# Kernel optimization log

Measured on AMD Instinct MI355X. Metric: run time of the kernel, lower is better.

The kernel has to match this reference:

```python
import jax, jax.numpy as jnp
import numpy as np

N, E, B = 100000, 3200000, 64   # nodes, edges, graphs
F_IN, F_OUT, N_OUT = 20, 20, 5


def setup_inputs() -> dict:
    key = jax.random.key(0)
    ks = jax.random.split(key, 9)
    x = jax.random.normal(ks[0], (N, F_IN), jnp.float32)
    edge_index = jax.random.randint(ks[1], (2, E), 0, N, dtype=jnp.int32)
    batch = jnp.sort(jax.random.randint(ks[2], (N,), 0, B, dtype=jnp.int32))
    s = 1.0 / np.sqrt(F_IN)
    W = jax.random.normal(ks[3], (F_IN, F_OUT), jnp.float32) * s       # GAT linear
    att_src = jax.random.normal(ks[4], (F_OUT,), jnp.float32) * s      # a_src (heads=1)
    att_dst = jax.random.normal(ks[5], (F_OUT,), jnp.float32) * s      # a_dst
    bias = jax.random.normal(ks[6], (F_OUT,), jnp.float32) * 0.01
    out_W = jax.random.normal(ks[7], (F_OUT, N_OUT), jnp.float32) * s
    out_b = jax.random.normal(ks[8], (N_OUT,), jnp.float32) * 0.01
    return {"x": x, "edge_index": edge_index, "batch": batch, "W": W,
            "att_src": att_src, "att_dst": att_dst, "bias": bias,
            "out_W": out_W, "out_b": out_b}


def reference(x, edge_index, batch, W, att_src, att_dst, bias, out_W, out_b):
    n = x.shape[0]
    # PyG GATConv default: add self-loops
    loop = jnp.arange(n, dtype=edge_index.dtype)
    src = jnp.concatenate([edge_index[0], loop])
    dst = jnp.concatenate([edge_index[1], loop])

    h = x @ W                                   # [N, F_OUT]
    a_s = h @ att_src                           # [N]
    a_d = h @ att_dst                           # [N]
    # per-edge attention logit, LeakyReLU(0.2) as in PyG GATConv
    e = jax.nn.leaky_relu(a_s[src] + a_d[dst], negative_slope=0.2)
    # segment softmax over incoming edges of each destination node
    m = jax.ops.segment_max(e, dst, num_segments=n)
    ex = jnp.exp(e - m[dst])
    den = jax.ops.segment_sum(ex, dst, num_segments=n)
    alpha = ex / den[dst]                       # [E+N]  (dropout inactive in eval)
    agg = jax.ops.segment_sum(alpha[:, None] * h[src], dst, num_segments=n) + bias

    xact = jax.nn.leaky_relu(agg, negative_slope=0.01)   # nn.LeakyReLU default
    # global mean pool per graph
    cnt = jax.ops.segment_sum(jnp.ones((n,), xact.dtype), batch, num_segments=B)
    pooled = jax.ops.segment_sum(xact, batch, num_segments=B) / jnp.maximum(cnt, 1.0)[:, None]
    logits = pooled @ out_W + out_b             # [B, 5]
    return jax.nn.softmax(logits, axis=-1)
```

## Files before the change

kernel.cpp:

```cpp
#include <hip/hip_runtime.h>
#include <math.h>

#define F_IN 20
#define F_OUT 20
#define N_OUT 5
#define NPB 128
#define NPB_SH 7
#define NBLK_A 256
#define HS 24
#define CAPMAX 5632
#define NBUCKMAX 800

__global__ __launch_bounds__(1024) void k1a_fused(
    const float* __restrict__ x, const float* __restrict__ W,
    const float* __restrict__ att_s, const float* __restrict__ att_d,
    float* __restrict__ hpack, float* __restrict__ a_d,
    const int* __restrict__ ei, int* __restrict__ gcur,
    unsigned int* __restrict__ bdata,
    int n, int E, int nbuck, int cap, int k1blocks)
{
    __shared__ float sW[F_IN * F_OUT];
    __shared__ float sas[F_OUT];
    __shared__ float sad[F_OUT];
    __shared__ int   sh[3 * NBUCKMAX];

    int tid = threadIdx.x;

    if (blockIdx.x < k1blocks) {
        for (int i = tid; i < F_IN * F_OUT; i += 1024) sW[i] = W[i];
        if (tid < F_OUT) { sas[tid] = att_s[tid]; sad[tid] = att_d[tid]; }
        __syncthreads();

        int i = blockIdx.x * 1024 + tid;
        if (i >= n) return;

        float xi[F_IN];
        const float4* xp = (const float4*)(x + (size_t)i * F_IN);
#pragma unroll
        for (int q = 0; q < F_IN / 4; ++q) {
            float4 v = xp[q];
            xi[4 * q + 0] = v.x; xi[4 * q + 1] = v.y;
            xi[4 * q + 2] = v.z; xi[4 * q + 3] = v.w;
        }

        float hrow[F_OUT];
        float as_acc = 0.f, ad_acc = 0.f;
#pragma unroll
        for (int j = 0; j < F_OUT; ++j) {
            float hj = 0.f;
#pragma unroll
            for (int k = 0; k < F_IN; ++k) hj += xi[k] * sW[k * F_OUT + j];
            hrow[j] = hj;
            as_acc += hj * sas[j];
            ad_acc += hj * sad[j];
        }

        float4* hp = (float4*)(hpack + (size_t)i * HS);
#pragma unroll
        for (int q = 0; q < F_OUT / 4; ++q) {
            float4 v;
            v.x = hrow[4 * q + 0]; v.y = hrow[4 * q + 1];
            v.z = hrow[4 * q + 2]; v.w = hrow[4 * q + 3];
            hp[q] = v;
        }
        float4 tail; tail.x = as_acc; tail.y = 0.f; tail.z = 0.f; tail.w = 0.f;
        hp[5] = tail;
        a_d[i] = ad_acc;
    } else {
        int bb   = blockIdx.x - k1blocks;
        int nbb  = gridDim.x - k1blocks;
        int* hist = sh;
        int* base = sh + nbuck;
        int* cur  = sh + 2 * nbuck;
        for (int b = tid; b < nbuck; b += 1024) { hist[b] = 0; cur[b] = 0; }
        __syncthreads();

        int chunk = (E + nbb - 1) / nbb;
        int start = bb * chunk;
        int end   = min(E, start + chunk);
        const int* dsts = ei + E;

        for (int e = start + tid; e < end; e += 1024)
            atomicAdd(&hist[dsts[e] >> NPB_SH], 1);
        __syncthreads();

        for (int b = tid; b < nbuck; b += 1024) {
            int c = hist[b];
            base[b] = c ? atomicAdd(&gcur[b], c) : 0;
        }
        __syncthreads();

        for (int e = start + tid; e < end; e += 1024) {
            int d = dsts[e];
            int s = ei[e];
            int b = d >> NPB_SH;
            int pos = base[b] + atomicAdd(&cur[b], 1);
            if (pos < cap)
                bdata[(size_t)b * cap + pos] =
                    ((unsigned)s << NPB_SH) | (unsigned)(d & (NPB - 1));
        }
    }
}

__global__ __launch_bounds__(512) void kb_srt(const int* __restrict__ gcur,
                                              const unsigned int* __restrict__ bdata,
                                              const float* __restrict__ hpack,
                                              const float* __restrict__ a_d,
                                              const float* __restrict__ bias,
                                              float* __restrict__ xact,
                                              int n, int cap)
{
    __shared__ int   sent[CAPMAX];
    __shared__ int   hist[NPB];
    __shared__ int   incl[NPB];
    __shared__ int   cur[NPB];
    __shared__ float adl[NPB];
    __shared__ float sbias[F_OUT];

    int b = blockIdx.x;
    int node_lo = b << NPB_SH;
    int nn = min(NPB, n - node_lo);
    int tid = threadIdx.x;

    if (tid < NPB) { hist[tid] = 0; cur[tid] = 0; }
    if (tid < nn) adl[tid] = a_d[node_lo + tid];
    if (tid < F_OUT) sbias[tid] = bias[tid];
    __syncthreads();

    int cnt = min(gcur[b], cap);
    const unsigned int* bd = bdata + (size_t)b * cap;

    for (int e = tid; e < cnt; e += 512)
        atomicAdd(&hist[bd[e] & (NPB - 1)], 1);
    __syncthreads();

    if (tid < NPB) incl[tid] = hist[tid];
    __syncthreads();
#pragma unroll
    for (int s = 1; s < NPB; s <<= 1) {
        int v = 0;
        if (tid < NPB && tid >= s) v = incl[tid - s];
        __syncthreads();
        if (tid < NPB) incl[tid] += v;
        __syncthreads();
    }

    for (int e = tid; e < cnt; e += 512) {
        unsigned w = bd[e];
        int ldst = (int)(w & (NPB - 1));
        int pos = incl[ldst] - hist[ldst] + atomicAdd(&cur[ldst], 1);
        sent[pos] = (int)(w >> NPB_SH);
    }
    __syncthreads();

    int node = tid >> 2, sub = tid & 3;
    float acc[21];
#pragma unroll
    for (int f = 0; f < 21; ++f) acc[f] = 0.f;

    if (node < nn) {
        int start = incl[node] - hist[node];
        int end   = incl[node];
        float ad  = adl[node];
        for (int k = start + sub; k < end; k += 4) {
            int src = sent[k];
            const float* row = hpack + (size_t)src * HS;
            const float4* hp = (const float4*)row;
            float as = row[20];
            float vv = as + ad;
            vv = vv > 0.f ? vv : 0.2f * vv;
            float ex = __expf(vv);
            float4 h0 = hp[0], h1 = hp[1], h2 = hp[2], h3 = hp[3], h4 = hp[4];
            acc[0]  += ex * h0.x; acc[1]  += ex * h0.y;
            acc[2]  += ex * h0.z; acc[3]  += ex * h0.w;
            acc[4]  += ex * h1.x; acc[5]  += ex * h1.y;
            acc[6]  += ex * h1.z; acc[7]  += ex * h1.w;
            acc[8]  += ex * h2.x; acc[9]  += ex * h2.y;
            acc[10] += ex * h2.z; acc[11] += ex * h2.w;
            acc[12] += ex * h3.x; acc[13] += ex * h3.y;
            acc[14] += ex * h3.z; acc[15] += ex * h3.w;
            acc[16] += ex * h4.x; acc[17] += ex * h4.y;
            acc[18] += ex * h4.z; acc[19] += ex * h4.w;
            acc[20] += ex;
        }
    }

#pragma unroll
    for (int f = 0; f < 21; ++f) {
        acc[f] += __shfl_xor(acc[f], 1);
        acc[f] += __shfl_xor(acc[f], 2);
    }

    if (node < nn && sub == 0) {
        int i = node_lo + node;
        const float* row = hpack + (size_t)i * HS;
        float vv = row[20] + adl[node];
        vv = vv > 0.f ? vv : 0.2f * vv;
        float exs = __expf(vv);
        float inv = 1.f / (acc[20] + exs);

        const float4* hp = (const float4*)row;
        float4* op = (float4*)(xact + (size_t)i * F_OUT);
#pragma unroll
        for (int q = 0; q < F_OUT / 4; ++q) {
            float4 hv = hp[q];
            float t0 = (acc[4 * q + 0] + exs * hv.x) * inv + sbias[4 * q + 0];
            float t1 = (acc[4 * q + 1] + exs * hv.y) * inv + sbias[4 * q + 1];
            float t2 = (acc[4 * q + 2] + exs * hv.z) * inv + sbias[4 * q + 2];
            float t3 = (acc[4 * q + 3] + exs * hv.w) * inv + sbias[4 * q + 3];
            float4 o;
            o.x = t0 > 0.f ? t0 : 0.01f * t0;
            o.y = t1 > 0.f ? t1 : 0.01f * t1;
            o.z = t2 > 0.f ? t2 : 0.01f * t2;
            o.w = t3 > 0.f ? t3 : 0.01f * t3;
            op[q] = o;
        }
    }
}

__global__ void k3_pool(const float* __restrict__ xact, const int* __restrict__ batch,
                        float* __restrict__ pooled, int n)
{
    int b = blockIdx.x;
    __shared__ int s_bounds[2];
    __shared__ float partial[4][F_OUT];
    if (threadIdx.x < 2) {
        int target = b + threadIdx.x;
        int lo = 0, hi = n;
        while (lo < hi) {
            int m = (lo + hi) >> 1;
            if (batch[m] < target) lo = m + 1; else hi = m;
        }
        s_bounds[threadIdx.x] = lo;
    }
    __syncthreads();
    int start = s_bounds[0], end = s_bounds[1];

    float acc[F_OUT];
#pragma unroll
    for (int f = 0; f < F_OUT; ++f) acc[f] = 0.f;

    for (int i = start + (int)threadIdx.x; i < end; i += (int)blockDim.x) {
        const float4* ap = (const float4*)(xact + (size_t)i * F_OUT);
#pragma unroll
        for (int q = 0; q < F_OUT / 4; ++q) {
            float4 v = ap[q];
            acc[4 * q + 0] += v.x;
            acc[4 * q + 1] += v.y;
            acc[4 * q + 2] += v.z;
            acc[4 * q + 3] += v.w;
        }
    }

#pragma unroll
    for (int f = 0; f < F_OUT; ++f) {
        float v = acc[f];
        v += __shfl_down(v, 32);
        v += __shfl_down(v, 16);
        v += __shfl_down(v, 8);
        v += __shfl_down(v, 4);
        v += __shfl_down(v, 2);
        v += __shfl_down(v, 1);
        acc[f] = v;
    }
    int wave = threadIdx.x >> 6, lane = threadIdx.x & 63;
    if (lane == 0) {
#pragma unroll
        for (int f = 0; f < F_OUT; ++f) partial[wave][f] = acc[f];
    }
    __syncthreads();
    if (threadIdx.x < F_OUT) {
        int f = threadIdx.x;
        float sum = partial[0][f] + partial[1][f] + partial[2][f] + partial[3][f];
        float cnt = (float)(end - start);
        cnt = cnt > 1.f ? cnt : 1.f;
        pooled[b * F_OUT + f] = sum / cnt;
    }
}

__global__ void k4_head(const float* __restrict__ pooled, const float* __restrict__ out_W,
                        const float* __restrict__ out_b, float* __restrict__ out, int B)
{
    int g = blockIdx.x * blockDim.x + threadIdx.x;
    if (g >= B) return;
    float p[F_OUT];
#pragma unroll
    for (int f = 0; f < F_OUT; ++f) p[f] = pooled[g * F_OUT + f];
    float lg[N_OUT];
#pragma unroll
    for (int o = 0; o < N_OUT; ++o) {
        float acc = out_b[o];
#pragma unroll
        for (int f = 0; f < F_OUT; ++f) acc += p[f] * out_W[f * N_OUT + o];
        lg[o] = acc;
    }
    float m = lg[0];
#pragma unroll
    for (int o = 1; o < N_OUT; ++o) m = lg[o] > m ? lg[o] : m;
    float s = 0.f;
#pragma unroll
    for (int o = 0; o < N_OUT; ++o) { lg[o] = expf(lg[o] - m); s += lg[o]; }
    float inv = 1.f / s;
#pragma unroll
    for (int o = 0; o < N_OUT; ++o) out[g * N_OUT + o] = lg[o] * inv;
}

extern "C" void kernel_launch(void* const* d_in, const int* in_sizes, int n_in,
                              void* d_out, int out_size, void* d_ws, size_t ws_size,
                              hipStream_t stream)
{
    const float* x       = (const float*)d_in[0];
    const int*   ei      = (const int*)  d_in[1];
    const int*   batch   = (const int*)  d_in[2];
    const float* W       = (const float*)d_in[3];
    const float* att_src = (const float*)d_in[4];
    const float* att_dst = (const float*)d_in[5];
    const float* bias    = (const float*)d_in[6];
    const float* out_W   = (const float*)d_in[7];
    const float* out_b   = (const float*)d_in[8];
    float* out = (float*)d_out;

    int n = in_sizes[0] / F_IN;
    int E = in_sizes[1] / 2;
    int B = out_size / N_OUT;

    int nbuck = (n + NPB - 1) >> NPB_SH;
    int avg   = E / nbuck;
    int cap   = avg + avg / 4 + 256;
    if (cap > CAPMAX) cap = CAPMAX;

    char* ws = (char*)d_ws;
    float* hpack  = (float*)ws;        ws += (size_t)n * HS * 4;
    float* a_d    = (float*)ws;        ws += (size_t)n * 4;
    float* xact   = (float*)ws;        ws += (size_t)n * F_OUT * 4;
    float* pooled = (float*)ws;        ws += (size_t)B * F_OUT * 4;
    int*   gcur   = (int*)ws;          ws += (size_t)nbuck * 4;
    ws = (char*)(((size_t)ws + 15) & ~(size_t)15);
    unsigned int* bdata = (unsigned int*)ws;  ws += (size_t)nbuck * cap * 4;

    hipMemsetAsync(gcur, 0, (size_t)nbuck * 4, stream);

    int k1blocks = (n + 1023) / 1024;

    k1a_fused<<<k1blocks + NBLK_A, 1024, 0, stream>>>(
        x, W, att_src, att_dst, hpack, a_d, ei, gcur, bdata,
        n, E, nbuck, cap, k1blocks);
    kb_srt   <<<nbuck, 512, 0, stream>>>(gcur, bdata, hpack, a_d, bias, xact, n, cap);
    k3_pool  <<<B, 256, 0, stream>>>(xact, batch, pooled, n);
    k4_head  <<<1, 64, 0, stream>>>(pooled, out_W, out_b, out, B);
}
```

Before: 202.3 us.

## Pack node features as bf16 and fuse mean-pooling into aggregation kernel

Node features h are stored as packed bf16 pairs with the fp32 source attention logit in a 64-byte row, down from a 96-byte fp32 row. This cuts the bytes fetched per edge in the random gather. The pooling kernel is removed: the aggregation kernel accumulates activations per graph in shared memory and atomically adds them to a global pooled buffer, and the head kernel divides by node counts. This drops the xact write and read-back and one launch, at the cost of bf16 rounding of h and nondeterministic float atomic ordering.

```diff
diff --git a/kernel.cpp b/kernel.cpp
--- a/kernel.cpp
+++ b/kernel.cpp
@@ -7,14 +7,25 @@
 #define NPB 128
 #define NPB_SH 7
 #define NBLK_A 256
-#define HS 24
+#define HSW 16
 #define CAPMAX 5632
 #define NBUCKMAX 800
+#define SPMAX 8
+
+__device__ __forceinline__ unsigned pack2bf(float a, float b) {
+    unsigned ua = __float_as_uint(a);
+    unsigned ub = __float_as_uint(b);
+    ua = (ua + 0x7fffu + ((ua >> 16) & 1u)) >> 16;
+    ub = ((ub + 0x7fffu + ((ub >> 16) & 1u)) >> 16) << 16;
+    return ua | ub;
+}
+#define BF2LO(u) __uint_as_float((u) << 16)
+#define BF2HI(u) __uint_as_float((u) & 0xffff0000u)
 
 __global__ __launch_bounds__(1024) void k1a_fused(
     const float* __restrict__ x, const float* __restrict__ W,
     const float* __restrict__ att_s, const float* __restrict__ att_d,
-    float* __restrict__ hpack, float* __restrict__ a_d,
+    unsigned* __restrict__ hpack, float* __restrict__ a_d,
     const int* __restrict__ ei, int* __restrict__ gcur,
     unsigned int* __restrict__ bdata,
     int n, int E, int nbuck, int cap, int k1blocks)
@@ -55,16 +66,21 @@
             ad_acc += hj * sad[j];
         }
 
-        float4* hp = (float4*)(hpack + (size_t)i * HS);
-#pragma unroll
-        for (int q = 0; q < F_OUT / 4; ++q) {
-            float4 v;
-            v.x = hrow[4 * q + 0]; v.y = hrow[4 * q + 1];
-            v.z = hrow[4 * q + 2]; v.w = hrow[4 * q + 3];
+        unsigned rw[HSW];
+#pragma unroll
+        for (int j = 0; j < 10; ++j) rw[j] = pack2bf(hrow[2 * j], hrow[2 * j + 1]);
+        rw[10] = __float_as_uint(as_acc);
+#pragma unroll
+        for (int j = 11; j < HSW; ++j) rw[j] = 0u;
+
+        uint4* hp = (uint4*)(hpack + (size_t)i * HSW);
+#pragma unroll
+        for (int q = 0; q < HSW / 4; ++q) {
+            uint4 v;
+            v.x = rw[4 * q + 0]; v.y = rw[4 * q + 1];
+            v.z = rw[4 * q + 2]; v.w = rw[4 * q + 3];
             hp[q] = v;
         }
-        float4 tail; tail.x = as_acc; tail.y = 0.f; tail.z = 0.f; tail.w = 0.f;
-        hp[5] = tail;
         a_d[i] = ad_acc;
     } else {
         int bb   = blockIdx.x - k1blocks;
@@ -104,10 +120,11 @@
 
 __global__ __launch_bounds__(512) void kb_srt(const int* __restrict__ gcur,
                                               const unsigned int* __restrict__ bdata,
-                                              const float* __restrict__ hpack,
+                                              const unsigned* __restrict__ hpack,
                                               const float* __restrict__ a_d,
                                               const float* __restrict__ bias,
-                                              float* __restrict__ xact,
+                                              const int* __restrict__ batch,
+                                              float* __restrict__ pooled,
                                               int n, int cap)
 {
     __shared__ int   sent[CAPMAX];
@@ -115,7 +132,9 @@
     __shared__ int   incl[NPB];
     __shared__ int   cur[NPB];
     __shared__ float adl[NPB];
+    __shared__ int   sbatch[NPB];
     __shared__ float sbias[F_OUT];
+    __shared__ float spool[SPMAX * F_OUT];
 
     int b = blockIdx.x;
     int node_lo = b << NPB_SH;
@@ -123,8 +142,12 @@
     int tid = threadIdx.x;
 
     if (tid < NPB) { hist[tid] = 0; cur[tid] = 0; }
-    if (tid < nn) adl[tid] = a_d[node_lo + tid];
+    if (tid < nn) {
+        adl[tid] = a_d[node_lo + tid];
+        sbatch[tid] = batch[node_lo + tid];
+    }
     if (tid < F_OUT) sbias[tid] = bias[tid];
+    if (tid < SPMAX * F_OUT) spool[tid] = 0.f;
     __syncthreads();
 
     int cnt = min(gcur[b], cap);
@@ -164,23 +187,22 @@
         float ad  = adl[node];
         for (int k = start + sub; k < end; k += 4) {
             int src = sent[k];
-            const float* row = hpack + (size_t)src * HS;
-            const float4* hp = (const float4*)row;
-            float as = row[20];
+            const uint4* rp = (const uint4*)(hpack + (size_t)src * HSW);
+            uint4 r0 = rp[0], r1 = rp[1], r2 = rp[2];
+            float as = __uint_as_float(r2.z);
             float vv = as + ad;
             vv = vv > 0.f ? vv : 0.2f * vv;
             float ex = __expf(vv);
-            float4 h0 = hp[0], h1 = hp[1], h2 = hp[2], h3 = hp[3], h4 = hp[4];
-            acc[0]  += ex * h0.x; acc[1]  += ex * h0.y;
-            acc[2]  += ex * h0.z; acc[3]  += ex * h0.w;
-            acc[4]  += ex * h1.x; acc[5]  += ex * h1.y;
-            acc[6]  += ex * h1.z; acc[7]  += ex * h1.w;
-            acc[8]  += ex * h2.x; acc[9]  += ex * h2.y;
-            acc[10] += ex * h2.z; acc[11] += ex * h2.w;
-            acc[12] += ex * h3.x; acc[13] += ex * h3.y;
-            acc[14] += ex * h3.z; acc[15] += ex * h3.w;
-            acc[16] += ex * h4.x; acc[17] += ex * h4.y;
-            acc[18] += ex * h4.z; acc[19] += ex * h4.w;
+            acc[0]  += ex * BF2LO(r0.x); acc[1]  += ex * BF2HI(r0.x);
+            acc[2]  += ex * BF2LO(r0.y); acc[3]  += ex * BF2HI(r0.y);
+            acc[4]  += ex * BF2LO(r0.z); acc[5]  += ex * BF2HI(r0.z);
+            acc[6]  += ex * BF2LO(r0.w); acc[7]  += ex * BF2HI(r0.w);
+            acc[8]  += ex * BF2LO(r1.x); acc[9]  += ex * BF2HI(r1.x);
+            acc[10] += ex * BF2LO(r1.y); acc[11] += ex * BF2HI(r1.y);
+            acc[12] += ex * BF2LO(r1.z); acc[13] += ex * BF2HI(r1.z);
+            acc[14] += ex * BF2LO(r1.w); acc[15] += ex * BF2HI(r1.w);
+            acc[16] += ex * BF2LO(r2.x); acc[17] += ex * BF2HI(r2.x);
+            acc[18] += ex * BF2LO(r2.y); acc[19] += ex * BF2HI(r2.y);
             acc[20] += ex;
         }
     }
@@ -193,99 +215,75 @@
 
     if (node < nn && sub == 0) {
         int i = node_lo + node;
-        const float* row = hpack + (size_t)i * HS;
-        float vv = row[20] + adl[node];
+        const uint4* rp = (const uint4*)(hpack + (size_t)i * HSW);
+        uint4 r0 = rp[0], r1 = rp[1], r2 = rp[2];
+        float vv = __uint_as_float(r2.z) + adl[node];
         vv = vv > 0.f ? vv : 0.2f * vv;
         float exs = __expf(vv);
         float inv = 1.f / (acc[20] + exs);
 
-        const float4* hp = (const float4*)row;
-        float4* op = (float4*)(xact + (size_t)i * F_OUT);
-#pragma unroll
-        for (int q = 0; q < F_OUT / 4; ++q) {
-            float4 hv = hp[q];
-            float t0 = (acc[4 * q + 0] + exs * hv.x) * inv + sbias[4 * q + 0];
-            float t1 = (acc[4 * q + 1] + exs * hv.y) * inv + sbias[4 * q + 1];
-            float t2 = (acc[4 * q + 2] + exs * hv.z) * inv + sbias[4 * q + 2];
-            float t3 = (acc[4 * q + 3] + exs * hv.w) * inv + sbias[4 * q + 3];
-            float4 o;
-            o.x = t0 > 0.f ? t0 : 0.01f * t0;
-            o.y = t1 > 0.f ? t1 : 0.01f * t1;
-            o.z = t2 > 0.f ? t2 : 0.01f * t2;
-            o.w = t3 > 0.f ? t3 : 0.01f * t3;
-            op[q] = o;
-        }
-    }
-}
-
-__global__ void k3_pool(const float* __restrict__ xact, const int* __restrict__ batch,
-                        float* __restrict__ pooled, int n)
+        float hs[F_OUT];
+        hs[0]  = BF2LO(r0.x); hs[1]  = BF2HI(r0.x);
+        hs[2]  = BF2LO(r0.y); hs[3]  = BF2HI(r0.y);
+        hs[4]  = BF2LO(r0.z); hs[5]  = BF2HI(r0.z);
+        hs[6]  = BF2LO(r0.w); hs[7]  = BF2HI(r0.w);
+        hs[8]  = BF2LO(r1.x); hs[9]  = BF2HI(r1.x);
+        hs[10] = BF2LO(r1.y); hs[11] = BF2HI(r1.y);
+        hs[12] = BF2LO(r1.z); hs[13] = BF2HI(r1.z);
+        hs[14] = BF2LO(r1.w); hs[15] = BF2HI(r1.w);
+        hs[16] = BF2LO(r2.x); hs[17] = BF2HI(r2.x);
+        hs[18] = BF2LO(r2.y); hs[19] = BF2HI(r2.y);
+
+        float v[F_OUT];
+#pragma unroll
+        for (int f = 0; f < F_OUT; ++f) {
+            float t = (acc[f] + exs * hs[f]) * inv + sbias[f];
+            v[f] = t > 0.f ? t : 0.01f * t;
+        }
+
+        int gl = sbatch[node] - sbatch[0];
+        if (gl < SPMAX) {
+#pragma unroll
+            for (int f = 0; f < F_OUT; ++f) atomicAdd(&spool[gl * F_OUT + f], v[f]);
+        } else {
+#pragma unroll
+            for (int f = 0; f < F_OUT; ++f)
+                atomicAdd(&pooled[(size_t)sbatch[node] * F_OUT + f], v[f]);
+        }
+    }
+    __syncthreads();
+
+    int g0 = sbatch[0];
+    int ngl = min(SPMAX, sbatch[nn - 1] - g0 + 1);
+    for (int idx = tid; idx < ngl * F_OUT; idx += 512)
+        atomicAdd(&pooled[(size_t)(g0 + idx / F_OUT) * F_OUT + idx % F_OUT], spool[idx]);
+}
+
+__global__ void k4_head(const float* __restrict__ pooled, const int* __restrict__ batch,
+                        const float* __restrict__ out_W, const float* __restrict__ out_b,
+                        float* __restrict__ out, int B, int n)
 {
-    int b = blockIdx.x;
-    __shared__ int s_bounds[2];
-    __shared__ float partial[4][F_OUT];
-    if (threadIdx.x < 2) {
-        int target = b + threadIdx.x;
+    int g = blockIdx.x * blockDim.x + threadIdx.x;
+    if (g >= B) return;
+
+    int bnd[2];
+#pragma unroll
+    for (int t = 0; t < 2; ++t) {
+        int target = g + t;
         int lo = 0, hi = n;
         while (lo < hi) {
             int m = (lo + hi) >> 1;
             if (batch[m] < target) lo = m + 1; else hi = m;
         }
-        s_bounds[threadIdx.x] = lo;
-    }
-    __syncthreads();
-    int start = s_bounds[0], end = s_bounds[1];
-
-    float acc[F_OUT];
-#pragma unroll
-    for (int f = 0; f < F_OUT; ++f) acc[f] = 0.f;
-
-    for (int i = start + (int)threadIdx.x; i < end; i += (int)blockDim.x) {
-        const float4* ap = (const float4*)(xact + (size_t)i * F_OUT);
-#pragma unroll
-        for (int q = 0; q < F_OUT / 4; ++q) {
-            float4 v = ap[q];
-            acc[4 * q + 0] += v.x;
-            acc[4 * q + 1] += v.y;
-            acc[4 * q + 2] += v.z;
-            acc[4 * q + 3] += v.w;
-        }
-    }
-
-#pragma unroll
-    for (int f = 0; f < F_OUT; ++f) {
-        float v = acc[f];
-        v += __shfl_down(v, 32);
-        v += __shfl_down(v, 16);
-        v += __shfl_down(v, 8);
-        v += __shfl_down(v, 4);
-        v += __shfl_down(v, 2);
-        v += __shfl_down(v, 1);
-        acc[f] = v;
-    }
-    int wave = threadIdx.x >> 6, lane = threadIdx.x & 63;
-    if (lane == 0) {
-#pragma unroll
-        for (int f = 0; f < F_OUT; ++f) partial[wave][f] = acc[f];
-    }
-    __syncthreads();
-    if (threadIdx.x < F_OUT) {
-        int f = threadIdx.x;
-        float sum = partial[0][f] + partial[1][f] + partial[2][f] + partial[3][f];
-        float cnt = (float)(end - start);
-        cnt = cnt > 1.f ? cnt : 1.f;
-        pooled[b * F_OUT + f] = sum / cnt;
-    }
-}
-
-__global__ void k4_head(const float* __restrict__ pooled, const float* __restrict__ out_W,
-                        const float* __restrict__ out_b, float* __restrict__ out, int B)
-{
-    int g = blockIdx.x * blockDim.x + threadIdx.x;
-    if (g >= B) return;
+        bnd[t] = lo;
+    }
+    float cntf = (float)(bnd[1] - bnd[0]);
+    float invc = 1.f / (cntf > 1.f ? cntf : 1.f);
+
     float p[F_OUT];
 #pragma unroll
-    for (int f = 0; f < F_OUT; ++f) p[f] = pooled[g * F_OUT + f];
+    for (int f = 0; f < F_OUT; ++f) p[f] = pooled[(size_t)g * F_OUT + f] * invc;
+
     float lg[N_OUT];
 #pragma unroll
     for (int o = 0; o < N_OUT; ++o) {
@@ -330,22 +328,21 @@
     if (cap > CAPMAX) cap = CAPMAX;
 
     char* ws = (char*)d_ws;
-    float* hpack  = (float*)ws;        ws += (size_t)n * HS * 4;
-    float* a_d    = (float*)ws;        ws += (size_t)n * 4;
-    float* xact   = (float*)ws;        ws += (size_t)n * F_OUT * 4;
-    float* pooled = (float*)ws;        ws += (size_t)B * F_OUT * 4;
-    int*   gcur   = (int*)ws;          ws += (size_t)nbuck * 4;
+    unsigned* hpack = (unsigned*)ws;   ws += (size_t)n * HSW * 4;
+    float* a_d      = (float*)ws;      ws += (size_t)n * 4;
+    int*   gcur     = (int*)ws;        ws += (size_t)nbuck * 4;
+    float* pooled   = (float*)ws;      ws += (size_t)B * F_OUT * 4;
     ws = (char*)(((size_t)ws + 15) & ~(size_t)15);
     unsigned int* bdata = (unsigned int*)ws;  ws += (size_t)nbuck * cap * 4;
 
-    hipMemsetAsync(gcur, 0, (size_t)nbuck * 4, stream);
+    hipMemsetAsync(gcur, 0, (size_t)nbuck * 4 + (size_t)B * F_OUT * 4, stream);
 
     int k1blocks = (n + 1023) / 1024;
 
     k1a_fused<<<k1blocks + NBLK_A, 1024, 0, stream>>>(
         x, W, att_src, att_dst, hpack, a_d, ei, gcur, bdata,
         n, E, nbuck, cap, k1blocks);
-    kb_srt   <<<nbuck, 512, 0, stream>>>(gcur, bdata, hpack, a_d, bias, xact, n, cap);
-    k3_pool  <<<B, 256, 0, stream>>>(xact, batch, pooled, n);
-    k4_head  <<<1, 64, 0, stream>>>(pooled, out_W, out_b, out, B);
-}
+    kb_srt   <<<nbuck, 512, 0, stream>>>(gcur, bdata, hpack, a_d, bias, batch,
+                                         pooled, n, cap);
+    k4_head  <<<1, 64, 0, stream>>>(pooled, batch, out_W, out_b, out, B, n);
+}
```

After: 197.9 us. -2.2%, faster.
